# Kernel optimization log

Hardware: AMD Instinct MI355X
Metric: run time of the kernel (lower is better)

The kernel has to match this reference:

```python
import jax, jax.numpy as jnp
import numpy as np

# dims
B, S, E, H = 2, 2048, 2048, 2688   # batch, seq, embedding_dim, hidden_dim
NH, DH = 4, 2688 // 4              # mLSTM heads, head dim
KS = 4                             # causal conv kernel size
BLK = 4                            # qkv_proj_blocksize
NPH = H // BLK                     # headwise-proj heads


def setup_inputs() -> dict:
    key = jax.random.key(0)
    ks = jax.random.split(key, 12)
    r = lambda i, shape, s=0.02: jax.random.normal(ks[i], shape, jnp.float32) * s
    return dict(
        x=jax.random.normal(ks[0], (B, S, E), jnp.float32),
        W_in=r(1, (E, 2 * H)),                       # up projection (no bias)
        conv_w=r(2, (KS, 1, H), 0.1),                # depthwise causal conv kernel (W, I/g, O)
        conv_b=jnp.zeros((H,), jnp.float32),
        Wq=r(3, (NPH, BLK, BLK), 0.3),               # headwise q proj
        Wk=r(4, (NPH, BLK, BLK), 0.3),               # headwise k proj
        Wv=r(5, (NPH, BLK, BLK), 0.3),               # headwise v proj
        W_ig=r(6, (3 * H, NH)),                      # input gate proj
        b_ig=jax.random.normal(ks[7], (NH,), jnp.float32),
        W_fg=r(8, (3 * H, NH)),                      # forget gate proj
        b_fg=jnp.linspace(3.0, 6.0, NH).astype(jnp.float32),
        norm_w=jnp.ones((H,), jnp.float32),          # multi-head layernorm weight
        skip=jnp.ones((H,), jnp.float32),            # learnable skip
        W_out=r(9, (H, E)),                          # down projection
    )


def _headwise(x, W):
    # LinearHeadwiseExpand: (B,S,H) -> (B,S,NPH,BLK) -> einsum -> (B,S,H)
    b, s, _ = x.shape
    xh = x.reshape(b, s, NPH, BLK)
    return jnp.einsum('bshd,hdo->bsho', xh, W).reshape(b, s, -1)


def reference(x, W_in, conv_w, conv_b, Wq, Wk, Wv, W_ig, b_ig, W_fg, b_fg, norm_w, skip, W_out):
    x_inner = x @ W_in                               # (B,S,2H)
    x_m, z = jnp.split(x_inner, 2, axis=-1)
    # depthwise causal conv1d
    xc = jax.lax.conv_general_dilated(
        x_m, conv_w, (1,), [(KS - 1, 0)],
        dimension_numbers=('NWC', 'WIO', 'NWC'), feature_group_count=H) + conv_b
    xca = jax.nn.silu(xc)
    q = _headwise(xca, Wq)
    k = _headwise(xca, Wk)
    v = _headwise(x_m, Wv)
    # ---- mLSTM cell (parallel stabilized form) ----
    qh = q.reshape(B, S, NH, DH).transpose(0, 2, 1, 3)   # (B,NH,S,DH)
    kh = k.reshape(B, S, NH, DH).transpose(0, 2, 1, 3)
    vh = v.reshape(B, S, NH, DH).transpose(0, 2, 1, 3)
    if_in = jnp.concatenate([q, k, v], axis=-1)          # (B,S,3H)
    i_pre = (if_in @ W_ig + b_ig).transpose(0, 2, 1)     # (B,NH,S)
    f_pre = (if_in @ W_fg + b_fg).transpose(0, 2, 1)
    log_fg = jax.nn.log_sigmoid(f_pre)                   # (B,NH,S)
    cs = jnp.cumsum(log_fg, axis=-1)
    # log decay matrix: sum of log forget gates t=j+1..i, causal masked
    dmat = cs[:, :, :, None] - cs[:, :, None, :]         # (B,NH,S,S)
    mask = jnp.tril(jnp.ones((S, S), bool))
    log_D = jnp.where(mask, dmat + i_pre[:, :, None, :], -jnp.inf)
    m = jnp.max(log_D, axis=-1, keepdims=True)           # stabilizer (B,NH,S,1)
    D = jnp.exp(log_D - m)
    qk = jnp.einsum('bnsd,bntd->bnst', qh, kh) / jnp.sqrt(jnp.float32(DH))
    C = qk * D
    n = jnp.maximum(jnp.abs(C.sum(-1, keepdims=True)), jnp.exp(-m))
    h = jnp.einsum('bnst,bntd->bnsd', C / (n + 1e-6), vh)
    # multi-head layernorm over DH, learnable scale over full H
    mu = h.mean(-1, keepdims=True)
    var = h.var(-1, keepdims=True)
    hn = (h - mu) * jax.lax.rsqrt(var + 1e-5)
    hn = hn.transpose(0, 2, 1, 3).reshape(B, S, H) * norm_w
    # ---- gated skip + output ----
    h_skip = hn + skip * xca
    hs = h_skip * jax.nn.silu(z)
    return hs @ W_out
```

## Files before the change

### kernel.cpp

```cpp
#include <hip/hip_runtime.h>

typedef unsigned short u16;
typedef unsigned int u32;
typedef __bf16 bf16x8 __attribute__((ext_vector_type(8)));
typedef float f32x4 __attribute__((ext_vector_type(4)));

#define BB   2
#define SS   2048
#define EE   2048
#define HH   2688
#define NHH  4
#define DHH  672
#define NPHH 672
#define H2   5376
#define H3   8064

__device__ __forceinline__ float b2f(u16 u) {
  union { unsigned int i; float f; } c; c.i = ((unsigned int)u) << 16; return c.f;
}
__device__ __forceinline__ u16 f2b(float f) {
  union { float f; unsigned int i; } c; c.f = f;
  unsigned int i = c.i;
  return (u16)((i + 0x7FFFu + ((i >> 16) & 1u)) >> 16);
}
__device__ __forceinline__ float silu_f(float x) { return x / (1.f + __expf(-x)); }
__device__ __forceinline__ float logsig_f(float f) {
  return (f >= 0.f) ? -log1pf(__expf(-f)) : (f - log1pf(__expf(f)));
}

__device__ __forceinline__ void gl2lds16(const u16* g, u16* s) {
  __builtin_amdgcn_global_load_lds(
      (const __attribute__((address_space(1))) u32*)g,
      (__attribute__((address_space(3))) u32*)s, 16, 0, 0);
}

template <int N> __device__ __forceinline__ void vmwait() {
  asm volatile("s_waitcnt vmcnt(%0)" :: "n"(N) : "memory");
}

template <int MODE, int OUTF32>
__global__ __launch_bounds__(512, 1) void gemm8(
    const u16* __restrict__ A, const u16* __restrict__ Bt, void* __restrict__ Cp,
    int M, int N, int K, int lda, int ldb, int ldc,
    long sAhi, long sAlo, long sBhi, long sBlo, long sChi, long sClo,
    const float* __restrict__ aux1, const float* __restrict__ aux2,
    int auxStride, int causal)
{
  constexpr int SLOT = (128 + 256) * 64;
  __shared__ __align__(16) u16 sm[3 * SLOT];

  int gx = gridDim.x;
  int nwg = gx * gridDim.y;
  int flat = blockIdx.y * gx + blockIdx.x;
  int qq = nwg >> 3, r8 = nwg & 7;
  int xcd = flat & 7, seq = flat >> 3;
  int logical = (xcd < r8 ? xcd * (qq + 1) : r8 * (qq + 1) + (xcd - r8) * qq) + seq;
  int bx = logical % gx, by = logical / gx;
  int m0 = by * 128, n0 = bx * 256;
  if (MODE == 1 && n0 > m0 + 127) return;

  int bz = blockIdx.z, bzh = bz >> 2, bzl = bz & 3;
  A  += bzh * sAhi + bzl * sAlo;
  Bt += bzh * sBhi + bzl * sBlo;
  const float* a1 = aux1 ? aux1 + (long)bz * auxStride : nullptr;
  const float* a2 = aux2 ? aux2 + (long)bz * auxStride : nullptr;
  u16*   C16 = (u16*)Cp + bzh * sChi + bzl * sClo;
  float* C32 = (float*)Cp + bzh * sChi + bzl * sClo;

  int t = threadIdx.x, lane = t & 63, w = t >> 6;
  int l15 = lane & 15, quad = lane >> 4;
  int wr = w >> 2, wc = w & 3;

  int srow = t >> 3;
  int sw8 = ((t & 7) ^ (srow & 7)) * 8;
  const u16* pS[6];
  int dOf[6];
#pragma unroll
  for (int c = 0; c < 2; ++c) {
    pS[c] = A + (long)(m0 + c * 64 + srow) * lda + sw8;
    dOf[c] = c * 4096 + w * 512;
  }
#pragma unroll
  for (int c = 0; c < 4; ++c) {
    pS[2 + c] = Bt + (long)(n0 + c * 64 + srow) * ldb + sw8;
    dOf[2 + c] = 8192 + c * 4096 + w * 512;
  }

  f32x4 acc[4][4];
#pragma unroll
  for (int i = 0; i < 4; i++)
#pragma unroll
    for (int j = 0; j < 4; j++) acc[i][j] = (f32x4){0.f, 0.f, 0.f, 0.f};

  int Keff = (MODE == 2 && causal) ? min(K, m0 + 128) : K;
  int T = Keff >> 6;

  auto STAGE = [&](int slot, int k2, int c) {
    gl2lds16(pS[c] + k2, sm + slot * SLOT + dOf[c]);
  };

  int npre = T < 2 ? T : 2;
  for (int tt = 0; tt < npre; ++tt)
#pragma unroll
    for (int c = 0; c < 6; ++c) STAGE(tt, tt << 6, c);
  if (npre >= 2) vmwait<6>(); else vmwait<0>();
  __builtin_amdgcn_s_barrier();
  __builtin_amdgcn_sched_barrier(0);

  int sl = 0;
  for (int tq = 0; tq < T; ++tq) {
    u16* Sb = sm + sl * SLOT;
    int sl2 = sl + 2; if (sl2 >= 3) sl2 -= 3;
    const bool stg = (tq + 2 < T);
    const int k2 = (tq + 2) << 6;
    int cx = (l15 & 7);

    bf16x8 bfr[4][2], af[2][2];
#pragma unroll
    for (int j = 0; j < 4; ++j)
#pragma unroll
      for (int ks = 0; ks < 2; ++ks)
        bfr[j][ks] = *reinterpret_cast<const bf16x8*>(
            Sb + 8192 + (wc * 64 + j * 16 + l15) * 64 + ((((ks << 2) + quad) ^ cx) << 3));
#pragma unroll
    for (int i = 0; i < 2; ++i)
#pragma unroll
      for (int ks = 0; ks < 2; ++ks)
        af[i][ks] = *reinterpret_cast<const bf16x8*>(
            Sb + (wr * 64 + i * 16 + l15) * 64 + ((((ks << 2) + quad) ^ cx) << 3));
    if (stg) { STAGE(sl2, k2, 0); STAGE(sl2, k2, 1); STAGE(sl2, k2, 2); }
    __builtin_amdgcn_s_barrier();
    asm volatile("s_waitcnt lgkmcnt(0)" ::: "memory");
    __builtin_amdgcn_sched_barrier(0);
    __builtin_amdgcn_s_setprio(1);
#pragma unroll
    for (int i = 0; i < 2; ++i)
#pragma unroll
      for (int j = 0; j < 4; ++j) {
        acc[i][j] = __builtin_amdgcn_mfma_f32_16x16x32_bf16(af[i][0], bfr[j][0], acc[i][j], 0, 0, 0);
        acc[i][j] = __builtin_amdgcn_mfma_f32_16x16x32_bf16(af[i][1], bfr[j][1], acc[i][j], 0, 0, 0);
      }
    __builtin_amdgcn_s_setprio(0);
    __builtin_amdgcn_sched_barrier(0);
    __builtin_amdgcn_s_barrier();

    bf16x8 ag[2][2];
#pragma unroll
    for (int i = 0; i < 2; ++i)
#pragma unroll
      for (int ks = 0; ks < 2; ++ks)
        ag[i][ks] = *reinterpret_cast<const bf16x8*>(
            Sb + (wr * 64 + (i + 2) * 16 + l15) * 64 + ((((ks << 2) + quad) ^ cx) << 3));
    if (stg) { STAGE(sl2, k2, 3); STAGE(sl2, k2, 4); STAGE(sl2, k2, 5); }
    __builtin_amdgcn_s_barrier();
    asm volatile("s_waitcnt lgkmcnt(0)" ::: "memory");
    __builtin_amdgcn_sched_barrier(0);
    __builtin_amdgcn_s_setprio(1);
#pragma unroll
    for (int i = 0; i < 2; ++i)
#pragma unroll
      for (int j = 0; j < 4; ++j) {
        acc[i + 2][j] = __builtin_amdgcn_mfma_f32_16x16x32_bf16(ag[i][0], bfr[j][0], acc[i + 2][j], 0, 0, 0);
        acc[i + 2][j] = __builtin_amdgcn_mfma_f32_16x16x32_bf16(ag[i][1], bfr[j][1], acc[i + 2][j], 0, 0, 0);
      }
    __builtin_amdgcn_s_setprio(0);
    __builtin_amdgcn_sched_barrier(0);
    if (tq + 1 < T) {
      if (stg) vmwait<6>(); else vmwait<0>();
      __builtin_amdgcn_s_barrier();
      __builtin_amdgcn_sched_barrier(0);
    }
    sl = sl + 1; if (sl >= 3) sl = 0;
  }

  const float rs = 0.03857583749f;
#pragma unroll
  for (int i = 0; i < 4; i++) {
#pragma unroll
    for (int j = 0; j < 4; j++) {
      int col = n0 + wc * 64 + j * 16 + l15;
      if (col >= N) continue;
#pragma unroll
      for (int rr = 0; rr < 4; rr++) {
        int row = m0 + wr * 64 + i * 16 + quad * 4 + rr;
        if (row >= M) continue;
        float v = acc[i][j][rr];
        if (MODE == 1) v = (col <= row) ? v * rs * __expf(a1[col] - a2[row]) : 0.f;
        else if (MODE == 2) v = v * a1[row];
        if (OUTF32) C32[(long)row * ldc + col] = v;
        else        C16[(long)row * ldc + col] = f2b(v);
      }
    }
  }
}

template <int BM, int MODE, int OUTF32>
__global__ __launch_bounds__(512, 1) void gemm_p(
    const u16* __restrict__ A, const u16* __restrict__ Bt, void* __restrict__ Cp,
    int M, int N, int K, int lda, int ldb, int ldc,
    long sAhi, long sAlo, long sBhi, long sBlo, long sChi, long sClo,
    const float* __restrict__ aux1, const float* __restrict__ aux2,
    int auxStride, int causal)
{
  constexpr int MFR   = BM / 32;
  constexpr int NPH   = MFR / 2;
  constexpr int SLOT  = (BM + 256) * 32;
  constexpr int ACH   = BM / 128;
  constexpr int LOADS = ACH + 2;
  __shared__ __align__(16) u16 sm[4 * SLOT];

  int gx = gridDim.x;
  int nwg = gx * gridDim.y;
  int flat = blockIdx.y * gx + blockIdx.x;
  int qq = nwg >> 3, r8 = nwg & 7;
  int xcd = flat & 7, seq = flat >> 3;
  int logical = (xcd < r8 ? xcd * (qq + 1) : r8 * (qq + 1) + (xcd - r8) * qq) + seq;
  int bx = logical % gx, by = logical / gx;
  int m0 = by * BM, n0 = bx * 256;
  if (MODE == 1 && n0 > m0 + BM - 1) return;

  int bz = blockIdx.z, bzh = bz >> 2, bzl = bz & 3;
  A  += bzh * sAhi + bzl * sAlo;
  Bt += bzh * sBhi + bzl * sBlo;
  const float* a1 = aux1 ? aux1 + (long)bz * auxStride : nullptr;
  const float* a2 = aux2 ? aux2 + (long)bz * auxStride : nullptr;
  u16*   C16 = (u16*)Cp + bzh * sChi + bzl * sClo;
  float* C32 = (float*)Cp + bzh * sChi + bzl * sClo;

  int t = threadIdx.x, lane = t & 63, w = t >> 6;
  int l15 = lane & 15, quad = lane >> 4;
  int wr = w >> 2, wc = w & 3;

  int srow = t >> 2;
  int swz = (((t & 3) ^ ((t >> 3) & 3)) * 8);
  const u16* pS[LOADS];
  int coff[LOADS];
#pragma unroll
  for (int c = 0; c < ACH; ++c) {
    pS[c] = A + (long)(m0 + c * 128 + srow) * lda + swz;
    coff[c] = c * 4096 + w * 512;
  }
#pragma unroll
  for (int c = 0; c < 2; ++c) {
    pS[ACH + c] = Bt + (long)(n0 + c * 128 + srow) * ldb + swz;
    coff[ACH + c] = BM * 32 + c * 4096 + w * 512;
  }

  int rswz = (quad ^ ((l15 >> 1) & 3)) * 8;
  int aoff = (wr * (BM / 2) + l15) * 32 + rswz;
  int boff = BM * 32 + (wc * 64 + l15) * 32 + rswz;

  f32x4 acc[MFR][4];
#pragma unroll
  for (int i = 0; i < MFR; i++)
#pragma unroll
    for (int j = 0; j < 4; j++) acc[i][j] = (f32x4){0.f, 0.f, 0.f, 0.f};

  int Keff = (MODE == 2 && causal) ? min(K, m0 + BM) : K;
  int T = Keff >> 5;

  auto STAGE1 = [&](int tt, int c) {
    gl2lds16(pS[c] + (tt << 5), sm + (tt & 3) * SLOT + coff[c]);
  };

  int npre = T < 3 ? T : 3;
  for (int tt = 0; tt < npre; ++tt)
#pragma unroll
    for (int c = 0; c < LOADS; ++c) STAGE1(tt, c);
  if (npre >= 3)      vmwait<2 * LOADS>();
  else if (npre == 2) vmwait<LOADS>();
  else                vmwait<0>();
  __builtin_amdgcn_s_barrier();
  __builtin_amdgcn_sched_barrier(0);

  for (int tq = 0; tq < T; ++tq) {
    u16* Sb = sm + (tq & 3) * SLOT;
    const bool stg = (tq + 3 < T);
    bf16x8 bf[4];
#pragma unroll
    for (int p = 0; p < NPH; ++p) {
      bf16x8 a0 = *reinterpret_cast<const bf16x8*>(Sb + aoff + (2 * p) * 512);
      bf16x8 a1v = *reinterpret_cast<const bf16x8*>(Sb + aoff + (2 * p + 1) * 512);
      if (p == 0) {
#pragma unroll
        for (int j = 0; j < 4; ++j)
          bf[j] = *reinterpret_cast<const bf16x8*>(Sb + boff + j * 512);
      }
      if (stg) {
#pragma unroll
        for (int c = p * LOADS / NPH; c < (p + 1) * LOADS / NPH; ++c)
          STAGE1(tq + 3, c);
      }
      __builtin_amdgcn_s_barrier();
      asm volatile("s_waitcnt lgkmcnt(0)" ::: "memory");
      __builtin_amdgcn_sched_barrier(0);
      __builtin_amdgcn_s_setprio(1);
#pragma unroll
      for (int j = 0; j < 4; ++j)
        acc[2 * p][j] = __builtin_amdgcn_mfma_f32_16x16x32_bf16(a0, bf[j], acc[2 * p][j], 0, 0, 0);
#pragma unroll
      for (int j = 0; j < 4; ++j)
        acc[2 * p + 1][j] = __builtin_amdgcn_mfma_f32_16x16x32_bf16(a1v, bf[j], acc[2 * p + 1][j], 0, 0, 0);
      __builtin_amdgcn_s_setprio(0);
      __builtin_amdgcn_sched_barrier(0);
    }
    if (tq + 1 < T) {
      if (tq + 3 < T)      vmwait<2 * LOADS>();
      else if (tq + 2 < T) vmwait<LOADS>();
      else                 vmwait<0>();
      __builtin_amdgcn_s_barrier();
      __builtin_amdgcn_sched_barrier(0);
    }
  }

  const float rs = 0.03857583749f;
#pragma unroll
  for (int i = 0; i < MFR; i++) {
#pragma unroll
    for (int j = 0; j < 4; j++) {
      int col = n0 + wc * 64 + j * 16 + l15;
      if (col >= N) continue;
#pragma unroll
      for (int rr = 0; rr < 4; rr++) {
        int row = m0 + wr * (BM / 2) + i * 16 + quad * 4 + rr;
        if (row >= M) continue;
        float v = acc[i][j][rr];
        if (MODE == 1) v = (col <= row) ? v * rs * __expf(a1[col] - a2[row]) : 0.f;
        else if (MODE == 2) v = v * a1[row];
        if (OUTF32) C32[(long)row * ldc + col] = v;
        else        C16[(long)row * ldc + col] = f2b(v);
      }
    }
  }
}

template <int F32IN>
__global__ __launch_bounds__(256) void transpose_any(
    const void* __restrict__ in, u16* __restrict__ out, int R, int C, int ldin,
    long inHi, long inLo, long outStride)
{
  __shared__ u16 tile[64][65];
  int bz = blockIdx.z, bzh = bz >> 2, bzl = bz & 3;
  const u16* in16 = (const u16*)in + bzh * inHi + bzl * inLo;
  const float* inf = (const float*)in + bzh * inHi + bzl * inLo;
  out += (long)bz * outStride;
  int r0 = blockIdx.y * 64, c0 = blockIdx.x * 64;
  int t = threadIdx.x;
  for (int idx = t; idx < 64 * 64; idx += 256) {
    int r = idx >> 6, c = idx & 63;
    int rr = r0 + r, cc = c0 + c;
    u16 v = 0;
    if (rr < R && cc < C) {
      long off = (long)rr * ldin + cc;
      v = F32IN ? f2b(inf[off]) : in16[off];
    }
    tile[r][c] = v;
  }
  __syncthreads();
  for (int idx = t; idx < 64 * 64; idx += 256) {
    int r = idx & 63, c = idx >> 6;
    int rr = r0 + r, cc = c0 + c;
    if (rr < R && cc < C) out[(long)cc * R + rr] = tile[r][c];
  }
}

__global__ __launch_bounds__(256) void convert_x(
    const float* __restrict__ x, u16* __restrict__ o)
{
  long i = ((long)blockIdx.x * 256 + threadIdx.x) * 8;
  if (i >= (long)4096 * EE) return;
  float4 a = *reinterpret_cast<const float4*>(x + i);
  float4 b = *reinterpret_cast<const float4*>(x + i + 4);
  u16 t8[8] = {f2b(a.x), f2b(a.y), f2b(a.z), f2b(a.w),
               f2b(b.x), f2b(b.y), f2b(b.z), f2b(b.w)};
  *reinterpret_cast<uint4*>(o + i) = *reinterpret_cast<uint4*>(t8);
}

__global__ __launch_bounds__(256) void prep_wt3(
    const float* __restrict__ Wig, const float* __restrict__ Wfg,
    u16* __restrict__ WT3)
{
  int i = blockIdx.x * 256 + threadIdx.x;
  if (i >= 128 * HH) return;
  int r = i / HH, c = i % HH;
  float v = 0.f;
  if (r < 24) {
    int seg = r >> 3, j = r & 7;
    const float* W = (j < 4) ? Wig : Wfg;
    v = W[(long)(seg * HH + c) * 4 + (j & 3)];
  }
  WT3[i] = f2b(v);
}

__global__ __launch_bounds__(256) void prep_wqkv(
    const float* __restrict__ Wq, const float* __restrict__ Wk,
    const float* __restrict__ Wv, u16* __restrict__ o)
{
  int i = blockIdx.x * 256 + threadIdx.x;
  if (i >= 3 * 10752) return;
  int m = i / 10752, j = i % 10752;
  const float* W = (m == 0) ? Wq : (m == 1) ? Wk : Wv;
  o[i] = f2b(W[j]);
}

__global__ __launch_bounds__(256) void conv_silu(
    const u16* __restrict__ xinner, const float* __restrict__ cw,
    const float* __restrict__ cb, u16* __restrict__ xca)
{
  long idx = (long)blockIdx.x * 256 + threadIdx.x;
  if (idx >= (long)BB * SS * HH / 4) return;
  int h4 = (int)(idx % (HH / 4)) * 4;
  long bs = idx / (HH / 4);
  int s = (int)(bs % SS);
  float4 acc = *reinterpret_cast<const float4*>(cb + h4);
#pragma unroll
  for (int w = 0; w < 4; w++) {
    int sp = s + w - 3;
    if (sp < 0) continue;
    uint2 xr = *reinterpret_cast<const uint2*>(xinner + (bs + w - 3) * H2 + h4);
    const u16* xh = (const u16*)&xr;
    float4 cwv = *reinterpret_cast<const float4*>(cw + w * HH + h4);
    acc.x += b2f(xh[0]) * cwv.x;
    acc.y += b2f(xh[1]) * cwv.y;
    acc.z += b2f(xh[2]) * cwv.z;
    acc.w += b2f(xh[3]) * cwv.w;
  }
  u16 o4[4] = {f2b(silu_f(acc.x)), f2b(silu_f(acc.y)),
               f2b(silu_f(acc.z)), f2b(silu_f(acc.w))};
  *reinterpret_cast<uint2*>(xca + bs * HH + h4) = *reinterpret_cast<uint2*>(o4);
}

__global__ __launch_bounds__(256) void headwise_qkv(
    const u16* __restrict__ xinner, const u16* __restrict__ xca,
    const u16* __restrict__ Wqkv,
    u16* __restrict__ q, u16* __restrict__ k, u16* __restrict__ v)
{
  int idx = blockIdx.x * 256 + threadIdx.x;
  if (idx >= BB * SS * NPHH) return;
  int nph = idx % NPHH;
  long bs = idx / NPHH;
  int cbase = nph * 4;
  uint2 xar = *reinterpret_cast<const uint2*>(xca + bs * HH + cbase);
  uint2 xmr = *reinterpret_cast<const uint2*>(xinner + bs * H2 + cbase);
  const u16* xa = (const u16*)&xar;
  const u16* xm = (const u16*)&xmr;
  float xaf[4], xmf[4];
#pragma unroll
  for (int d = 0; d < 4; d++) { xaf[d] = b2f(xa[d]); xmf[d] = b2f(xm[d]); }
  union { uint4 v4[2]; u16 h[16]; } wq, wk, wv;
  const uint4* wqp = reinterpret_cast<const uint4*>(Wqkv + nph * 16);
  const uint4* wkp = reinterpret_cast<const uint4*>(Wqkv + 10752 + nph * 16);
  const uint4* wvp = reinterpret_cast<const uint4*>(Wqkv + 21504 + nph * 16);
  wq.v4[0] = wqp[0]; wq.v4[1] = wqp[1];
  wk.v4[0] = wkp[0]; wk.v4[1] = wkp[1];
  wv.v4[0] = wvp[0]; wv.v4[1] = wvp[1];
  u16 qo[4], ko[4], vo[4];
#pragma unroll
  for (int o = 0; o < 4; o++) {
    float aq = 0.f, ak = 0.f, av = 0.f;
#pragma unroll
    for (int d = 0; d < 4; d++) {
      aq += xaf[d] * b2f(wq.h[d * 4 + o]);
      ak += xaf[d] * b2f(wk.h[d * 4 + o]);
      av += xmf[d] * b2f(wv.h[d * 4 + o]);
    }
    qo[o] = f2b(aq); ko[o] = f2b(ak); vo[o] = f2b(av);
  }
  long ob = bs * HH + cbase;
  *reinterpret_cast<uint2*>(q + ob) = *reinterpret_cast<uint2*>(qo);
  *reinterpret_cast<uint2*>(k + ob) = *reinterpret_cast<uint2*>(ko);
  *reinterpret_cast<uint2*>(v + ob) = *reinterpret_cast<uint2*>(vo);
}

__global__ __launch_bounds__(1024) void scan_kernel(
    const float* __restrict__ G, const float* __restrict__ big,
    const float* __restrict__ bfg,
    float* __restrict__ avec, float* __restrict__ rmaxvec, float* __restrict__ mvec)
{
  __shared__ float buf[2][SS];
  __shared__ float isave[SS];
  __shared__ float cssave[SS];
  int bn = blockIdx.x;
  int b = bn >> 2, n = bn & 3;
  int t = threadIdx.x;
  float bi = big[n], bf = bfg[n];
  for (int i = t; i < SS; i += 1024) {
    long tk = (long)b * SS + i;
    float ip = G[tk * 24 + n] + G[(4096 + tk) * 24 + 8 + n] +
               G[(8192 + tk) * 24 + 16 + n] + bi;
    float fp = G[tk * 24 + 4 + n] + G[(4096 + tk) * 24 + 12 + n] +
               G[(8192 + tk) * 24 + 20 + n] + bf;
    isave[i] = ip;
    buf[0][i] = logsig_f(fp);
  }
  __syncthreads();
  int src = 0;
  for (int off = 1; off < SS; off <<= 1) {
    int dst = 1 - src;
    for (int i = t; i < SS; i += 1024) {
      float x = buf[src][i];
      if (i >= off) x += buf[src][i - off];
      buf[dst][i] = x;
    }
    __syncthreads();
    src = dst;
  }
  for (int i = t; i < SS; i += 1024) {
    float cs = buf[src][i];
    cssave[i] = cs;
    float a = isave[i] - cs;
    avec[(long)bn * SS + i] = a;
    buf[src][i] = a;
  }
  __syncthreads();
  for (int off = 1; off < SS; off <<= 1) {
    int dst = 1 - src;
    for (int i = t; i < SS; i += 1024) {
      float x = buf[src][i];
      if (i >= off) x = fmaxf(x, buf[src][i - off]);
      buf[dst][i] = x;
    }
    __syncthreads();
    src = dst;
  }
  for (int i = t; i < SS; i += 1024) {
    rmaxvec[(long)bn * SS + i] = buf[src][i];
    mvec[(long)bn * SS + i] = cssave[i] + buf[src][i];
  }
}

__global__ __launch_bounds__(256) void rowsum_kernel(
    const u16* __restrict__ P, const float* __restrict__ mvec, float* __restrict__ invn,
    long Pstride)
{
  int bz = blockIdx.z;
  P += (long)bz * Pstride;
  mvec += (long)bz * SS;
  invn += (long)bz * SS;
  int row = (blockIdx.x * 256 + threadIdx.x) >> 6;
  int lane = threadIdx.x & 63;
  if (row >= SS) return;
  const u16* pr = P + (long)row * SS;
  float s = 0.f;
  int j0 = lane * 8;
  for (; j0 + 7 <= row; j0 += 512) {
    uint4 u = *reinterpret_cast<const uint4*>(pr + j0);
    const u16* e = (const u16*)&u;
#pragma unroll
    for (int q = 0; q < 8; ++q) s += b2f(e[q]);
  }
  if (j0 <= row) {
    for (int q = 0; j0 + q <= row; ++q) s += b2f(pr[j0 + q]);
  }
#pragma unroll
  for (int off = 32; off > 0; off >>= 1) s += __shfl_down(s, off);
  if (lane == 0) {
    float n = fmaxf(fabsf(s), __expf(-mvec[row]));
    invn[row] = 1.f / (n + 1e-6f);
  }
}

__global__ __launch_bounds__(256) void ln_skip_gate(
    const u16* __restrict__ h, const u16* __restrict__ xca,
    const u16* __restrict__ xinner, const float* __restrict__ normw,
    const float* __restrict__ skipw, u16* __restrict__ hs)
{
  int row = (blockIdx.x * 256 + threadIdx.x) >> 6;
  int lane = threadIdx.x & 63;
  if (row >= BB * NHH * SS) return;
  int s = row % SS;
  int n = (row / SS) % NHH;
  int b = row / (SS * NHH);
  const u16* hr = h + (long)row * DHH;
  float sum = 0.f, ss = 0.f;
  float vx[6], vy[6];
#pragma unroll
  for (int i = 0; i < 6; ++i) {
    int d2 = lane + i * 64;
    float x = 0.f, y = 0.f;
    if (d2 < DHH / 2) {
      u32 u = *reinterpret_cast<const u32*>(hr + d2 * 2);
      x = b2f((u16)u); y = b2f((u16)(u >> 16));
    }
    vx[i] = x; vy[i] = y;
    sum += x + y; ss += x * x + y * y;
  }
#pragma unroll
  for (int off = 32; off > 0; off >>= 1) { sum += __shfl_down(sum, off); ss += __shfl_down(ss, off); }
  sum = __shfl(sum, 0); ss = __shfl(ss, 0);
  float mu = sum / (float)DHH;
  float var = ss / (float)DHH - mu * mu;
  float rstd = rsqrtf(var + 1e-5f);
  long bs = (long)b * SS + s;
#pragma unroll
  for (int i = 0; i < 6; ++i) {
    int d2 = lane + i * 64;
    if (d2 >= DHH / 2) continue;
    int c = n * DHH + d2 * 2;
    float2 nw = *reinterpret_cast<const float2*>(normw + c);
    float2 sw = *reinterpret_cast<const float2*>(skipw + c);
    u32 xcu = *reinterpret_cast<const u32*>(xca + bs * HH + c);
    u32 zu  = *reinterpret_cast<const u32*>(xinner + bs * H2 + HH + c);
    float h0 = (vx[i] - mu) * rstd * nw.x + sw.x * b2f((u16)xcu);
    float h1 = (vy[i] - mu) * rstd * nw.y + sw.y * b2f((u16)(xcu >> 16));
    float o0 = h0 * silu_f(b2f((u16)zu));
    float o1 = h1 * silu_f(b2f((u16)(zu >> 16)));
    u32 ou = (u32)f2b(o0) | ((u32)f2b(o1) << 16);
    *reinterpret_cast<u32*>(hs + bs * HH + c) = ou;
  }
}

__global__ __launch_bounds__(256) void fill_sentinel(float* out, float v, long n) {
  long i = (long)blockIdx.x * 256 + threadIdx.x;
  if (i < n) out[i] = v;
}

extern "C" void kernel_launch(void* const* d_in, const int* in_sizes, int n_in,
                              void* d_out, int out_size, void* d_ws, size_t ws_size,
                              hipStream_t stream)
{
  const float* x      = (const float*)d_in[0];
  const float* W_in   = (const float*)d_in[1];
  const float* conv_w = (const float*)d_in[2];
  const float* conv_b = (const float*)d_in[3];
  const float* Wq     = (const float*)d_in[4];
  const float* Wk     = (const float*)d_in[5];
  const float* Wv     = (const float*)d_in[6];
  const float* W_ig   = (const float*)d_in[7];
  const float* b_ig   = (const float*)d_in[8];
  const float* W_fg   = (const float*)d_in[9];
  const float* b_fg   = (const float*)d_in[10];
  const float* norm_w = (const float*)d_in[11];
  const float* skipw  = (const float*)d_in[12];
  const float* W_out  = (const float*)d_in[13];
  float* out = (float*)d_out;
  const long SD = (long)SS * DHH;
  const long SP = (long)SS * SS;
  const long BH = (long)SS * HH;

  u16* ws = (u16*)d_ws;
  size_t off = 0;
  auto alloc = [&](size_t n) { u16* p = ws + off; off += n; return p; };
  u16* x_inner = alloc((size_t)4096 * H2);
  u16* xca     = alloc((size_t)4096 * HH);
  u16* qb      = alloc((size_t)4096 * HH);
  u16* kb      = alloc((size_t)4096 * HH);
  u16* vb      = alloc((size_t)4096 * HH);
  float* fvec  = (float*)(ws + off);
  off += 4 * 16384 * 2;
  float* avec    = fvec;
  float* rmaxvec = avec + 16384;
  float* mvec    = rmaxvec + 16384;
  float* invn    = mvec + 16384;
  u16* vt8 = alloc((size_t)8 * SD);
  u16* Pb8 = alloc((size_t)8 * SP);
  size_t need = off * 2;
  long outn = (long)4096 * EE;

  if (ws_size < need) {
    fill_sentinel<<<dim3((outn + 255) / 256), 256, 0, stream>>>(
        out, 200.f + 0.01f * (float)(ws_size >> 20), outn);
    return;
  }

  u16* W_inT  = qb;
  u16* xbf    = kb;
  u16* W_outT = vb;
  u16* hbuf   = kb;
  u16* hsbuf  = qb;
  u16* WT3    = Pb8;
  float* G    = (float*)(Pb8 + 344064);
  u16* Wqkv   = Pb8 + 933888;

  prep_wt3<<<dim3(1344, 1, 1), 256, 0, stream>>>(W_ig, W_fg, WT3);
  prep_wqkv<<<dim3(126, 1, 1), 256, 0, stream>>>(Wq, Wk, Wv, Wqkv);
  transpose_any<1><<<dim3(84, 32, 1), 256, 0, stream>>>(
      W_in, W_inT, EE, H2, H2, 0, 0, 0);
  convert_x<<<dim3(4096, 1, 1), 256, 0, stream>>>(x, xbf);
  gemm8<0, 0><<<dim3(21, 32, 1), 512, 0, stream>>>(
      xbf, W_inT, x_inner, 4096, H2, EE, EE, EE, H2,
      0, 0, 0, 0, 0, 0, nullptr, nullptr, 0, 0);
  conv_silu<<<dim3(10752, 1, 1), 256, 0, stream>>>(x_inner, conv_w, conv_b, xca);
  headwise_qkv<<<dim3(10752, 1, 1), 256, 0, stream>>>(
      x_inner, xca, Wqkv, qb, kb, vb);
  gemm8<0, 1><<<dim3(1, 96, 1), 512, 0, stream>>>(
      qb, WT3, G, 12288, 24, HH, HH, HH, 24,
      0, 0, 0, 0, 0, 0, nullptr, nullptr, 0, 0);
  scan_kernel<<<dim3(8, 1, 1), 1024, 0, stream>>>(G, b_ig, b_fg, avec, rmaxvec, mvec);
  transpose_any<0><<<dim3(11, 32, 8), 256, 0, stream>>>(
      vb, vt8, SS, DHH, HH, BH, DHH, SD);
  gemm_p<256, 1, 0><<<dim3(8, 8, 8), 512, 0, stream>>>(
      qb, kb, Pb8, SS, SS, DHH, HH, HH, SS,
      BH, DHH, BH, DHH, 4 * SP, SP, avec, rmaxvec, SS, 0);
  rowsum_kernel<<<dim3(512, 1, 8), 256, 0, stream>>>(Pb8, mvec, invn, SP);
  gemm8<2, 0><<<dim3(3, 16, 8), 512, 0, stream>>>(
      Pb8, vt8, hbuf, SS, DHH, SS, SS, SS, DHH,
      4 * SP, SP, 4 * SD, SD, 4 * SD, SD, invn, nullptr, SS, 1);
  transpose_any<1><<<dim3(32, 42, 1), 256, 0, stream>>>(
      W_out, W_outT, HH, EE, EE, 0, 0, 0);
  ln_skip_gate<<<dim3(4096, 1, 1), 256, 0, stream>>>(
      hbuf, xca, x_inner, norm_w, skipw, hsbuf);
  gemm8<0, 1><<<dim3(8, 32, 1), 512, 0, stream>>>(
      hsbuf, W_outT, out, 4096, EE, HH, HH, HH, EE,
      0, 0, 0, 0, 0, 0, nullptr, nullptr, 0, 0);
}
```

Before: 661.8 us.

## Add 256x256-tile GEMM kernel for the up-projection

Measured after the change: 692.9 us. 4.7% more time.

```diff
diff --git a/kernel.cpp b/kernel.cpp
--- a/kernel.cpp
+++ b/kernel.cpp
@@ -36,6 +36,146 @@
 
 template <int N> __device__ __forceinline__ void vmwait() {
   asm volatile("s_waitcnt vmcnt(%0)" :: "n"(N) : "memory");
+}
+
+template <int MODE, int OUTF32>
+__global__ __launch_bounds__(512, 1) void gemm256(
+    const u16* __restrict__ A, const u16* __restrict__ Bt, void* __restrict__ Cp,
+    int M, int N, int K, int lda, int ldb, int ldc,
+    long sAhi, long sAlo, long sBhi, long sBlo, long sChi, long sClo,
+    const float* __restrict__ aux1, const float* __restrict__ aux2,
+    int auxStride, int causal)
+{
+  __shared__ __align__(16) u16 sm[2 * 32768];
+
+  int gx = gridDim.x;
+  int nwg = gx * gridDim.y;
+  int flat = blockIdx.y * gx + blockIdx.x;
+  int qq = nwg >> 3, r8 = nwg & 7;
+  int xcd = flat & 7, seq = flat >> 3;
+  int logical = (xcd < r8 ? xcd * (qq + 1) : r8 * (qq + 1) + (xcd - r8) * qq) + seq;
+  int bx = logical % gx, by = logical / gx;
+  int m0 = by * 256, n0 = bx * 256;
+  if (MODE == 1 && n0 > m0 + 255) return;
+
+  int bz = blockIdx.z, bzh = bz >> 2, bzl = bz & 3;
+  A  += bzh * sAhi + bzl * sAlo;
+  Bt += bzh * sBhi + bzl * sBlo;
+  const float* a1 = aux1 ? aux1 + (long)bz * auxStride : nullptr;
+  const float* a2 = aux2 ? aux2 + (long)bz * auxStride : nullptr;
+  u16*   C16 = (u16*)Cp + bzh * sChi + bzl * sClo;
+  float* C32 = (float*)Cp + bzh * sChi + bzl * sClo;
+
+  int t = threadIdx.x, lane = t & 63, w = t >> 6;
+  int l15 = lane & 15, quad = lane >> 4;
+  int wr = w >> 2, wc = w & 3;
+  int cx = l15 & 7;
+
+  int srow = t >> 3;
+  int sw8 = ((t & 7) ^ (srow & 7)) * 8;
+  const u16* pA = A + (long)(m0 + srow) * lda + sw8;
+  const u16* pB = Bt + (long)(n0 + srow) * ldb + sw8;
+
+  f32x4 acc[8][4];
+#pragma unroll
+  for (int i = 0; i < 8; i++)
+#pragma unroll
+    for (int j = 0; j < 4; j++) acc[i][j] = (f32x4){0.f, 0.f, 0.f, 0.f};
+
+  int Keff = (MODE == 2 && causal) ? min(K, m0 + 256) : K;
+  int T = Keff >> 6;
+
+  auto SA = [&](int buf, int h, int tt) {
+    int k2 = tt << 6;
+    u16* d = sm + buf * 32768 + h * 8192 + w * 512;
+    gl2lds16(pA + (long)(h * 128) * lda + k2, d);
+    gl2lds16(pA + (long)(h * 128 + 64) * lda + k2, d + 4096);
+  };
+  auto SB = [&](int buf, int h, int tt) {
+    int k2 = tt << 6;
+    u16* d = sm + buf * 32768 + 16384 + h * 8192 + w * 512;
+    gl2lds16(pB + (long)(h * 128) * ldb + k2, d);
+    gl2lds16(pB + (long)(h * 128 + 64) * ldb + k2, d + 4096);
+  };
+
+  SA(0, 0, 0); SA(0, 1, 0); SB(0, 0, 0); SB(0, 1, 0);
+  if (T > 1) { SB(1, 0, 1); SB(1, 1, 1); vmwait<4>(); }
+  else vmwait<0>();
+  __builtin_amdgcn_s_barrier();
+  __builtin_amdgcn_sched_barrier(0);
+
+  for (int tq = 0; tq < T; ++tq) {
+    u16* Sb = sm + (tq & 1) * 32768;
+    int nb = (tq + 1) & 1;
+    bf16x8 bfr[4][2];
+
+#pragma unroll
+    for (int p = 0; p < 4; ++p) {
+      bf16x8 a0, a1v;
+      a0  = *reinterpret_cast<const bf16x8*>(
+          Sb + (wr * 128 + (2 * p) * 16 + l15) * 64 + ((quad ^ cx) << 3));
+      a1v = *reinterpret_cast<const bf16x8*>(
+          Sb + (wr * 128 + (2 * p + 1) * 16 + l15) * 64 + ((quad ^ cx) << 3));
+      bf16x8 a0h, a1h;
+      a0h = *reinterpret_cast<const bf16x8*>(
+          Sb + (wr * 128 + (2 * p) * 16 + l15) * 64 + (((4 + quad) ^ cx) << 3));
+      a1h = *reinterpret_cast<const bf16x8*>(
+          Sb + (wr * 128 + (2 * p + 1) * 16 + l15) * 64 + (((4 + quad) ^ cx) << 3));
+      if (p == 0) {
+#pragma unroll
+        for (int j = 0; j < 4; ++j) {
+          bfr[j][0] = *reinterpret_cast<const bf16x8*>(
+              Sb + 16384 + (wc * 64 + j * 16 + l15) * 64 + ((quad ^ cx) << 3));
+          bfr[j][1] = *reinterpret_cast<const bf16x8*>(
+              Sb + 16384 + (wc * 64 + j * 16 + l15) * 64 + (((4 + quad) ^ cx) << 3));
+        }
+      }
+      if (p == 0) { if (tq + 1 < T) SA(nb, 0, tq + 1); }
+      else if (p == 1) { if (tq + 1 < T) SA(nb, 1, tq + 1); }
+      else if (p == 2) { if (tq + 2 < T) SB(tq & 1, 0, tq + 2); }
+      else { if (tq + 2 < T) SB(tq & 1, 1, tq + 2); }
+
+      __builtin_amdgcn_s_barrier();
+      asm volatile("s_waitcnt lgkmcnt(0)" ::: "memory");
+      __builtin_amdgcn_sched_barrier(0);
+      __builtin_amdgcn_s_setprio(1);
+#pragma unroll
+      for (int j = 0; j < 4; ++j) {
+        acc[2 * p][j] = __builtin_amdgcn_mfma_f32_16x16x32_bf16(a0, bfr[j][0], acc[2 * p][j], 0, 0, 0);
+        acc[2 * p][j] = __builtin_amdgcn_mfma_f32_16x16x32_bf16(a0h, bfr[j][1], acc[2 * p][j], 0, 0, 0);
+        acc[2 * p + 1][j] = __builtin_amdgcn_mfma_f32_16x16x32_bf16(a1v, bfr[j][0], acc[2 * p + 1][j], 0, 0, 0);
+        acc[2 * p + 1][j] = __builtin_amdgcn_mfma_f32_16x16x32_bf16(a1h, bfr[j][1], acc[2 * p + 1][j], 0, 0, 0);
+      }
+      __builtin_amdgcn_s_setprio(0);
+      __builtin_amdgcn_sched_barrier(0);
+      __builtin_amdgcn_s_barrier();
+    }
+    if (tq + 1 < T) {
+      if (tq + 2 < T) vmwait<4>(); else vmwait<0>();
+      __builtin_amdgcn_s_barrier();
+      __builtin_amdgcn_sched_barrier(0);
+    }
+  }
+
+  const float rs = 0.03857583749f;
+#pragma unroll
+  for (int i = 0; i < 8; i++) {
+#pragma unroll
+    for (int j = 0; j < 4; j++) {
+      int col = n0 + wc * 64 + j * 16 + l15;
+      if (col >= N) continue;
+#pragma unroll
+      for (int rr = 0; rr < 4; rr++) {
+        int row = m0 + wr * 128 + i * 16 + quad * 4 + rr;
+        if (row >= M) continue;
+        float v = acc[i][j][rr];
+        if (MODE == 1) v = (col <= row) ? v * rs * __expf(a1[col] - a2[row]) : 0.f;
+        else if (MODE == 2) v = v * a1[row];
+        if (OUTF32) C32[(long)row * ldc + col] = v;
+        else        C16[(long)row * ldc + col] = f2b(v);
+      }
+    }
+  }
 }
 
 template <int MODE, int OUTF32>
@@ -677,7 +817,7 @@
   transpose_any<1><<<dim3(84, 32, 1), 256, 0, stream>>>(
       W_in, W_inT, EE, H2, H2, 0, 0, 0);
   convert_x<<<dim3(4096, 1, 1), 256, 0, stream>>>(x, xbf);
-  gemm8<0, 0><<<dim3(21, 32, 1), 512, 0, stream>>>(
+  gemm256<0, 0><<<dim3(21, 16, 1), 512, 0, stream>>>(
       xbf, W_inT, x_inner, 4096, H2, EE, EE, EE, H2,
       0, 0, 0, 0, 0, 0, nullptr, nullptr, 0, 0);
   conv_silu<<<dim3(10752, 1, 1), 256, 0, stream>>>(x_inner, conv_w, conv_b, xca);
```

## Fuse conv+SiLU with headwise qkv and replace gate GEMM with GEMV kernel

Applied to the files above, without the earlier changes.

New measurement: 651.5 us. Within noise of the previous version (-1.6%).

```diff
diff --git a/kernel.cpp b/kernel.cpp
--- a/kernel.cpp
+++ b/kernel.cpp
@@ -376,22 +376,6 @@
   *reinterpret_cast<uint4*>(o + i) = *reinterpret_cast<uint4*>(t8);
 }
 
-__global__ __launch_bounds__(256) void prep_wt3(
-    const float* __restrict__ Wig, const float* __restrict__ Wfg,
-    u16* __restrict__ WT3)
-{
-  int i = blockIdx.x * 256 + threadIdx.x;
-  if (i >= 128 * HH) return;
-  int r = i / HH, c = i % HH;
-  float v = 0.f;
-  if (r < 24) {
-    int seg = r >> 3, j = r & 7;
-    const float* W = (j < 4) ? Wig : Wfg;
-    v = W[(long)(seg * HH + c) * 4 + (j & 3)];
-  }
-  WT3[i] = f2b(v);
-}
-
 __global__ __launch_bounds__(256) void prep_wqkv(
     const float* __restrict__ Wq, const float* __restrict__ Wk,
     const float* __restrict__ Wv, u16* __restrict__ o)
@@ -403,21 +387,26 @@
   o[i] = f2b(W[j]);
 }
 
-__global__ __launch_bounds__(256) void conv_silu(
+__global__ __launch_bounds__(256) void conv_head(
     const u16* __restrict__ xinner, const float* __restrict__ cw,
-    const float* __restrict__ cb, u16* __restrict__ xca)
+    const float* __restrict__ cb, const u16* __restrict__ Wqkv,
+    u16* __restrict__ xca, u16* __restrict__ q, u16* __restrict__ k,
+    u16* __restrict__ v)
 {
   long idx = (long)blockIdx.x * 256 + threadIdx.x;
-  if (idx >= (long)BB * SS * HH / 4) return;
-  int h4 = (int)(idx % (HH / 4)) * 4;
-  long bs = idx / (HH / 4);
+  if (idx >= (long)BB * SS * NPHH) return;
+  int nph = (int)(idx % NPHH);
+  long bs = idx / NPHH;
   int s = (int)(bs % SS);
+  int h4 = nph * 4;
   float4 acc = *reinterpret_cast<const float4*>(cb + h4);
+  uint2 xmr;
 #pragma unroll
   for (int w = 0; w < 4; w++) {
     int sp = s + w - 3;
     if (sp < 0) continue;
     uint2 xr = *reinterpret_cast<const uint2*>(xinner + (bs + w - 3) * H2 + h4);
+    if (w == 3) xmr = xr;
     const u16* xh = (const u16*)&xr;
     float4 cwv = *reinterpret_cast<const float4*>(cw + w * HH + h4);
     acc.x += b2f(xh[0]) * cwv.x;
@@ -425,28 +414,16 @@
     acc.z += b2f(xh[2]) * cwv.z;
     acc.w += b2f(xh[3]) * cwv.w;
   }
-  u16 o4[4] = {f2b(silu_f(acc.x)), f2b(silu_f(acc.y)),
-               f2b(silu_f(acc.z)), f2b(silu_f(acc.w))};
-  *reinterpret_cast<uint2*>(xca + bs * HH + h4) = *reinterpret_cast<uint2*>(o4);
-}
-
-__global__ __launch_bounds__(256) void headwise_qkv(
-    const u16* __restrict__ xinner, const u16* __restrict__ xca,
-    const u16* __restrict__ Wqkv,
-    u16* __restrict__ q, u16* __restrict__ k, u16* __restrict__ v)
-{
-  int idx = blockIdx.x * 256 + threadIdx.x;
-  if (idx >= BB * SS * NPHH) return;
-  int nph = idx % NPHH;
-  long bs = idx / NPHH;
-  int cbase = nph * 4;
-  uint2 xar = *reinterpret_cast<const uint2*>(xca + bs * HH + cbase);
-  uint2 xmr = *reinterpret_cast<const uint2*>(xinner + bs * H2 + cbase);
-  const u16* xa = (const u16*)&xar;
+  float xaf[4] = {silu_f(acc.x), silu_f(acc.y), silu_f(acc.z), silu_f(acc.w)};
+  u16 xa16[4] = {f2b(xaf[0]), f2b(xaf[1]), f2b(xaf[2]), f2b(xaf[3])};
+#pragma unroll
+  for (int d = 0; d < 4; d++) xaf[d] = b2f(xa16[d]);
   const u16* xm = (const u16*)&xmr;
-  float xaf[4], xmf[4];
-#pragma unroll
-  for (int d = 0; d < 4; d++) { xaf[d] = b2f(xa[d]); xmf[d] = b2f(xm[d]); }
+  float xmf[4];
+#pragma unroll
+  for (int d = 0; d < 4; d++) xmf[d] = b2f(xm[d]);
+  *reinterpret_cast<uint2*>(xca + bs * HH + h4) = *reinterpret_cast<uint2*>(xa16);
+
   union { uint4 v4[2]; u16 h[16]; } wq, wk, wv;
   const uint4* wqp = reinterpret_cast<const uint4*>(Wqkv + nph * 16);
   const uint4* wkp = reinterpret_cast<const uint4*>(Wqkv + 10752 + nph * 16);
@@ -466,10 +443,68 @@
     }
     qo[o] = f2b(aq); ko[o] = f2b(ak); vo[o] = f2b(av);
   }
-  long ob = bs * HH + cbase;
+  long ob = bs * HH + h4;
   *reinterpret_cast<uint2*>(q + ob) = *reinterpret_cast<uint2*>(qo);
   *reinterpret_cast<uint2*>(k + ob) = *reinterpret_cast<uint2*>(ko);
   *reinterpret_cast<uint2*>(v + ob) = *reinterpret_cast<uint2*>(vo);
+}
+
+__global__ __launch_bounds__(256) void gate_gemv(
+    const u16* __restrict__ qb, const u16* __restrict__ kb,
+    const u16* __restrict__ vb, const float* __restrict__ Wig,
+    const float* __restrict__ Wfg, float* __restrict__ G)
+{
+  __shared__ u16 wlds[8 * HH];
+  int seg = blockIdx.y;
+  const u16* X = (seg == 0) ? qb : (seg == 1) ? kb : vb;
+  int t = threadIdx.x;
+  for (int c = t; c < HH; c += 256) {
+    float4 wi = *reinterpret_cast<const float4*>(Wig + ((long)seg * HH + c) * 4);
+    float4 wf = *reinterpret_cast<const float4*>(Wfg + ((long)seg * HH + c) * 4);
+    wlds[0 * HH + c] = f2b(wi.x); wlds[1 * HH + c] = f2b(wi.y);
+    wlds[2 * HH + c] = f2b(wi.z); wlds[3 * HH + c] = f2b(wi.w);
+    wlds[4 * HH + c] = f2b(wf.x); wlds[5 * HH + c] = f2b(wf.y);
+    wlds[6 * HH + c] = f2b(wf.z); wlds[7 * HH + c] = f2b(wf.w);
+  }
+  __syncthreads();
+  int wv = t >> 6, lane = t & 63;
+  int r0 = blockIdx.x * 32 + wv * 8;
+  for (int r = 0; r < 8; ++r) {
+    int row = r0 + r;
+    const u16* xr = X + (long)row * HH;
+    float a0=0,a1=0,a2=0,a3=0,a4=0,a5=0,a6=0,a7=0;
+    for (int ch = lane; ch < HH / 8; ch += 64) {
+      uint4 xv = *reinterpret_cast<const uint4*>(xr + ch * 8);
+      const u16* xe = (const u16*)&xv;
+      float xf[8];
+#pragma unroll
+      for (int e = 0; e < 8; ++e) xf[e] = b2f(xe[e]);
+#pragma unroll
+      for (int j = 0; j < 8; ++j) {
+        uint4 wv4 = *reinterpret_cast<const uint4*>(wlds + j * HH + ch * 8);
+        const u16* we = (const u16*)&wv4;
+        float s = 0.f;
+#pragma unroll
+        for (int e = 0; e < 8; ++e) s += xf[e] * b2f(we[e]);
+        if (j == 0) a0 += s; else if (j == 1) a1 += s;
+        else if (j == 2) a2 += s; else if (j == 3) a3 += s;
+        else if (j == 4) a4 += s; else if (j == 5) a5 += s;
+        else if (j == 6) a6 += s; else a7 += s;
+      }
+    }
+#pragma unroll
+    for (int off = 32; off > 0; off >>= 1) {
+      a0 += __shfl_down(a0, off); a1 += __shfl_down(a1, off);
+      a2 += __shfl_down(a2, off); a3 += __shfl_down(a3, off);
+      a4 += __shfl_down(a4, off); a5 += __shfl_down(a5, off);
+      a6 += __shfl_down(a6, off); a7 += __shfl_down(a7, off);
+    }
+    if (lane == 0) {
+      float* g = G + ((long)seg * 4096 + row) * 24 + seg * 8;
+      g[0] = a0; g[1] = a1; g[2] = a2; g[3] = a3;
+      g[4] = a4; g[5] = a5; g[6] = a6; g[7] = a7;
+    }
+  }
 }
 
 __global__ __launch_bounds__(1024) void scan_kernel(
@@ -668,11 +703,9 @@
   u16* W_outT = vb;
   u16* hbuf   = kb;
   u16* hsbuf  = qb;
-  u16* WT3    = Pb8;
   float* G    = (float*)(Pb8 + 344064);
   u16* Wqkv   = Pb8 + 933888;
 
-  prep_wt3<<<dim3(1344, 1, 1), 256, 0, stream>>>(W_ig, W_fg, WT3);
   prep_wqkv<<<dim3(126, 1, 1), 256, 0, stream>>>(Wq, Wk, Wv, Wqkv);
   transpose_any<1><<<dim3(84, 32, 1), 256, 0, stream>>>(
       W_in, W_inT, EE, H2, H2, 0, 0, 0);
@@ -680,12 +713,9 @@
   gemm8<0, 0><<<dim3(21, 32, 1), 512, 0, stream>>>(
       xbf, W_inT, x_inner, 4096, H2, EE, EE, EE, H2,
       0, 0, 0, 0, 0, 0, nullptr, nullptr, 0, 0);
-  conv_silu<<<dim3(10752, 1, 1), 256, 0, stream>>>(x_inner, conv_w, conv_b, xca);
-  headwise_qkv<<<dim3(10752, 1, 1), 256, 0, stream>>>(
-      x_inner, xca, Wqkv, qb, kb, vb);
-  gemm8<0, 1><<<dim3(1, 96, 1), 512, 0, stream>>>(
-      qb, WT3, G, 12288, 24, HH, HH, HH, 24,
-      0, 0, 0, 0, 0, 0, nullptr, nullptr, 0, 0);
+  conv_head<<<dim3(10752, 1, 1), 256, 0, stream>>>(
+      x_inner, conv_w, conv_b, Wqkv, xca, qb, kb, vb);
+  gate_gemv<<<dim3(128, 3, 1), 256, 0, stream>>>(qb, kb, vb, W_ig, W_fg, G);
   scan_kernel<<<dim3(8, 1, 1), 1024, 0, stream>>>(G, b_ig, b_fg, avec, rmaxvec, mvec);
   transpose_any<0><<<dim3(11, 32, 8), 256, 0, stream>>>(
       vb, vt8, SS, DHH, HH, BH, DHH, SD);
```
